# Kernel tuning notes

Hardware: AMD Instinct MI355X
Metric: run time of the kernel (lower is better)

## Reference

```python
import jax, jax.numpy as jnp
import numpy as np
import math

H = 12
DH = 64
MAX_POS = 1024

def setup_inputs() -> dict:
    key = jax.random.key(0)
    ks = jax.random.split(key, 8)
    B, L, D = 2, 1024, 768
    s = 0.02
    return {
        "hidden_states": jax.random.normal(ks[0], (B, L, D), jnp.float32),
        "attention_mask": jnp.zeros((B, 1, 1, L), jnp.float32),
        "struct_matrix": jax.random.uniform(ks[1], (5, B, 1, L, L), jnp.float32),
        "Wq": jax.random.normal(ks[2], (D, D), jnp.float32) * s,
        "bq": jnp.zeros((D,), jnp.float32),
        "Wk": jax.random.normal(ks[3], (D, D), jnp.float32) * s,
        "bk": jnp.zeros((D,), jnp.float32),
        "Wv": jax.random.normal(ks[4], (D, D), jnp.float32) * s,
        "bv": jnp.zeros((D,), jnp.float32),
        "dist_emb": jax.random.normal(ks[5], (2 * MAX_POS - 1, DH), jnp.float32) * s,
        "ssan_w": jax.random.normal(ks[6], (5, H, DH, DH), jnp.float32) * s,
        "abs_bias": jnp.zeros((5, H), jnp.float32),
    }

def reference(hidden_states, attention_mask, struct_matrix, Wq, bq, Wk, bk, Wv, bv, dist_emb, ssan_w, abs_bias):
    B, L, D = hidden_states.shape

    def heads(x):  # [B,L,D] -> [B,H,L,dh]
        return x.reshape(B, L, H, DH).transpose(0, 2, 1, 3)

    q = heads(hidden_states @ Wq + bq)
    k = heads(hidden_states @ Wk + bk)
    v = heads(hidden_states @ Wv + bv)

    scores = jnp.einsum('bhqd,bhkd->bhqk', q, k)

    # relative_key_query positional scores
    pos_ids = jnp.arange(L)
    distance = pos_ids[:, None] - pos_ids[None, :]          # [L,L]
    pos = dist_emb[distance + MAX_POS - 1]                  # [L,L,dh]
    scores = scores + jnp.einsum('bhld,lrd->bhlr', q, pos)
    scores = scores + jnp.einsum('bhrd,lrd->bhlr', k, pos)

    scores = scores / math.sqrt(DH)
    scores = scores + attention_mask

    # 5 SSAN bilinear bias terms, masked by structural matrices
    for i in range(5):
        bias = jnp.einsum('bhqd,hde,bhke->bhqk', q, ssan_w[i], k)
        scores = scores + (bias + abs_bias[i][None, :, None, None]) * struct_matrix[i]

    probs = jax.nn.softmax(scores, axis=-1)
    ctx = jnp.einsum('bhqk,bhkd->bqhd', probs, v).reshape(B, L, D)
    return ctx
```

## Files before the change

kernel.cpp:

```cpp
#include <hip/hip_runtime.h>
#include <math.h>

#define NB 2
#define NL 1024
#define ND 768
#define NH 12
#define DH 64

typedef _Float16 f16;
typedef _Float16 f16x2 __attribute__((ext_vector_type(2)));
typedef _Float16 f16x4 __attribute__((ext_vector_type(4)));
typedef _Float16 f16x8 __attribute__((ext_vector_type(8)));
typedef float f32x4 __attribute__((ext_vector_type(4)));

#define MFMA16(a, b, c) __builtin_amdgcn_mfma_f32_16x16x32_f16((a), (b), (c), 0, 0, 0)

__device__ __forceinline__ void soft_barrier() {
    asm volatile("s_waitcnt lgkmcnt(0)\n\ts_barrier" ::: "memory");
}

__global__ __launch_bounds__(256) void prep_kernel(
    const float* __restrict__ hs,
    const float* __restrict__ Wq, const float* __restrict__ Wk,
    const float* __restrict__ Wv, const float* __restrict__ sw,
    const float* __restrict__ de,
    f16* __restrict__ hsf, f16* __restrict__ wt, f16* __restrict__ swt,
    f16* __restrict__ de16)
{
    __shared__ float sT[64 * 66];
    const int t = threadIdx.x;
    const int tile = blockIdx.x;

    if (tile < 768) {
        const int base = tile * 2048 + t * 8;
        float4 a = *(const float4*)&hs[base];
        float4 b = *(const float4*)&hs[base + 4];
        f16x8 hv;
        hv[0] = (f16)a.x; hv[1] = (f16)a.y; hv[2] = (f16)a.z; hv[3] = (f16)a.w;
        hv[4] = (f16)b.x; hv[5] = (f16)b.y; hv[6] = (f16)b.z; hv[7] = (f16)b.w;
        *(f16x8*)&hsf[base] = hv;
        return;
    }
    if (tile >= 1260) {
        const int base = (tile - 1260) * 2048 + t * 8;
        if (base < 2047 * 64) {
            float4 a = *(const float4*)&de[base];
            float4 b = *(const float4*)&de[base + 4];
            f16x8 hv;
            hv[0] = (f16)a.x; hv[1] = (f16)a.y; hv[2] = (f16)a.z; hv[3] = (f16)a.w;
            hv[4] = (f16)b.x; hv[5] = (f16)b.y; hv[6] = (f16)b.z; hv[7] = (f16)b.w;
            *(f16x8*)&de16[base] = hv;
        }
        return;
    }

    const float* S; f16* D; int sRS, dRS;
    const int ti = tile - 768;
    if (ti < 432) {
        const int mat = ti / 144, r2 = ti % 144, ht = r2 / 12, kt = r2 % 12;
        const float* W = (mat == 0) ? Wq : (mat == 1) ? Wk : Wv;
        S = W + (size_t)(kt * 64) * ND + ht * 64;
        D = wt + (size_t)((mat * NH + ht) * 64) * ND + kt * 64;
        sRS = ND; dRS = ND;
    } else {
        const int i = ti - 432;
        S = sw + (size_t)i * 4096;
        D = swt + (size_t)i * 4096;
        sRS = 64; dRS = 64;
    }

    {
        const int kk = t >> 2, nb = (t & 3) * 16;
        float v[16];
        #pragma unroll
        for (int j = 0; j < 4; ++j)
            *(float4*)&v[4 * j] = *(const float4*)&S[(size_t)kk * sRS + nb + 4 * j];
        #pragma unroll
        for (int jj = 0; jj < 16; ++jj)
            sT[(nb + jj) * 66 + kk] = v[jj];
    }
    soft_barrier();
    {
        const int n = t >> 2, kb = (t & 3) * 16;
        f16 tmp[16];
        #pragma unroll
        for (int j = 0; j < 8; ++j) {
            float2 x = *(float2*)&sT[n * 66 + kb + 2 * j];
            tmp[2 * j]     = (f16)x.x;
            tmp[2 * j + 1] = (f16)x.y;
        }
        *(f16x8*)&D[(size_t)n * dRS + kb]     = *(f16x8*)&tmp[0];
        *(f16x8*)&D[(size_t)n * dRS + kb + 8] = *(f16x8*)&tmp[8];
    }
}

__global__ __launch_bounds__(256, 4) void qkv_kernel(
    const f16* __restrict__ hsf, const f16* __restrict__ wt,
    const float* __restrict__ bq, const float* __restrict__ bk,
    const float* __restrict__ bv,
    f16* __restrict__ qf, f16* __restrict__ kf, f16* __restrict__ vt)
{
    __shared__ f16 sA[64 * 72], sB[64 * 72];
    __shared__ float sT[64 * 66];

    const int m0  = blockIdx.x * 64;
    const int y   = blockIdx.y;
    const int mat = y / NH, h = y % NH;
    const int t = threadIdx.x, lane = t & 63, w = t >> 6;
    const int quad = lane >> 4, l15 = lane & 15;
    const int wm = w >> 1, wn = w & 1;

    const float* bias = (mat == 0) ? bq : (mat == 1) ? bk : bv;

    f32x4 acc[2][2];
    #pragma unroll
    for (int r = 0; r < 2; ++r)
        #pragma unroll
        for (int c = 0; c < 2; ++c) acc[r][c] = (f32x4){0.f, 0.f, 0.f, 0.f};

    const int srow = t >> 2, scol = (t & 3) * 16;
    const f16* Ag = hsf + (size_t)(m0 + srow) * ND + scol;
    const f16* Bg = wt + ((size_t)y * 64 + srow) * ND + scol;

    for (int k0 = 0; k0 < ND; k0 += 64) {
        soft_barrier();
        *(f16x8*)&sA[srow * 72 + scol]     = *(const f16x8*)&Ag[k0];
        *(f16x8*)&sA[srow * 72 + scol + 8] = *(const f16x8*)&Ag[k0 + 8];
        *(f16x8*)&sB[srow * 72 + scol]     = *(const f16x8*)&Bg[k0];
        *(f16x8*)&sB[srow * 72 + scol + 8] = *(const f16x8*)&Bg[k0 + 8];
        soft_barrier();
        #pragma unroll
        for (int kk = 0; kk < 64; kk += 32) {
            const int ko = kk + quad * 8;
            f16x8 a0 = *(f16x8*)&sA[(32 * wm + l15) * 72 + ko];
            f16x8 a1 = *(f16x8*)&sA[(32 * wm + 16 + l15) * 72 + ko];
            f16x8 b0 = *(f16x8*)&sB[(32 * wn + l15) * 72 + ko];
            f16x8 b1 = *(f16x8*)&sB[(32 * wn + 16 + l15) * 72 + ko];
            acc[0][0] = MFMA16(a0, b0, acc[0][0]);
            acc[0][1] = MFMA16(a0, b1, acc[0][1]);
            acc[1][0] = MFMA16(a1, b0, acc[1][0]);
            acc[1][1] = MFMA16(a1, b1, acc[1][1]);
        }
    }
    soft_barrier();

    const int bb = m0 >> 10;
    const int lbase = m0 & 1023;
    const int bh = bb * NH + h;

    if (mat < 2) {
        #pragma unroll
        for (int r = 0; r < 2; ++r)
            #pragma unroll
            for (int c = 0; c < 2; ++c) {
                const int col = 32 * wn + 16 * c + l15;
                const float bz = bias[h * 64 + col];
                #pragma unroll
                for (int rr = 0; rr < 4; ++rr)
                    sT[(32 * wm + 16 * r + 4 * quad + rr) * 66 + col] = acc[r][c][rr] + bz;
            }
        soft_barrier();
        const int orow = t >> 2, ocb = (t & 3) * 16;
        f16 tmp[16];
        #pragma unroll
        for (int j = 0; j < 8; ++j) {
            float2 x = *(float2*)&sT[orow * 66 + ocb + 2 * j];
            tmp[2 * j] = (f16)x.x; tmp[2 * j + 1] = (f16)x.y;
        }
        f16* dst = ((mat == 0) ? qf : kf) + ((size_t)bh * NL + lbase + orow) * DH + ocb;
        *(f16x8*)dst       = *(f16x8*)&tmp[0];
        *(f16x8*)(dst + 8) = *(f16x8*)&tmp[8];
    } else {
        #pragma unroll
        for (int r = 0; r < 2; ++r)
            #pragma unroll
            for (int c = 0; c < 2; ++c) {
                const int col = 32 * wn + 16 * c + l15;
                const float bz = bias[h * 64 + col];
                #pragma unroll
                for (int rr = 0; rr < 4; ++rr)
                    sT[col * 66 + 32 * wm + 16 * r + 4 * quad + rr] = acc[r][c][rr] + bz;
            }
        soft_barrier();
        const int d = t >> 2, lcb = (t & 3) * 16;
        f16 tmp[16];
        #pragma unroll
        for (int j = 0; j < 8; ++j) {
            float2 x = *(float2*)&sT[d * 66 + lcb + 2 * j];
            tmp[2 * j] = (f16)x.x; tmp[2 * j + 1] = (f16)x.y;
        }
        f16* dst = vt + ((size_t)bh * DH + d) * NL + lbase + lcb;
        *(f16x8*)dst       = *(f16x8*)&tmp[0];
        *(f16x8*)(dst + 8) = *(f16x8*)&tmp[8];
    }
}

__global__ __launch_bounds__(256, 2) void attn_kernel(
    const f16* __restrict__ qf, const f16* __restrict__ kf,
    const f16* __restrict__ vt, const f16* __restrict__ swt,
    const float* __restrict__ mask, const float* __restrict__ struct_m,
    const f16* __restrict__ de16, const float* __restrict__ abs_bias,
    float* __restrict__ out)
{
    __shared__ f16 sK[64 * 72];
    __shared__ f16 sVt[2][64 * 72];
    __shared__ f16 sE[96 * 72];
    __shared__ f16 sQEl[96 * 34];
    __shared__ f16 sKEl[96 * 34];
    __shared__ float sS[32 * 68];
    __shared__ f16 sP[32 * 72];
    __shared__ float sAlpha[32], sL[32];

    const int l0 = blockIdx.x * 32;
    const int bh = blockIdx.y;
    const int bb = bh / NH, h = bh % NH;
    const int t  = threadIdx.x;
    const int lane  = t & 63;
    const int w     = t >> 6;
    const int quad  = lane >> 4;
    const int l15   = lane & 15;
    const int msub  = w >> 1;
    const int npair = w & 1;

    f16x8 aQ[2], aW[5][2];
    {
        const size_t qrow = ((size_t)bh * NL + l0 + 16 * msub + l15) * DH;
        #pragma unroll
        for (int K = 0; K < 2; ++K)
            aQ[K] = *(const f16x8*)&qf[qrow + 32 * K + 8 * quad];
    }

    {
        #pragma unroll
        for (int b = 0; b < 2; ++b) {
            const int pb0  = (b == 0) ? 0 : 3;
            const int pcnt = (b == 0) ? 3 : 2;
            #pragma unroll
            for (int pi = 0; pi < 3; ++pi) {
                if (pi < pcnt) {
                    const int p = pb0 + pi;
                    const f16* Wp = swt + ((size_t)(p * NH + h)) * 64 * 64;
                    #pragma unroll
                    for (int ntl = 0; ntl < 2; ++ntl) {
                        const int nt = 2 * npair + ntl;
                        f32x4 c = (f32x4){0.f, 0.f, 0.f, 0.f};
                        #pragma unroll
                        for (int K = 0; K < 2; ++K) {
                            f16x8 bw = *(const f16x8*)&Wp[(size_t)(16 * nt + l15) * 64 + 32 * K + 8 * quad];
                            c = MFMA16(aQ[K], bw, c);
                        }
                        #pragma unroll
                        for (int r = 0; r < 4; ++r)
                            sE[(pi * 32 + 16 * msub + 4 * quad + r) * 72 + 16 * nt + l15] = (f16)c[r];
                    }
                }
            }
            soft_barrier();
            #pragma unroll
            for (int pi = 0; pi < 3; ++pi) {
                if (pi < pcnt) {
                    #pragma unroll
                    for (int K = 0; K < 2; ++K)
                        aW[pb0 + pi][K] =
                            *(const f16x8*)&sE[(pi * 32 + 16 * msub + l15) * 72 + 32 * K + 8 * quad];
                }
            }
            soft_barrier();
        }
    }

    float ab[5];
    #pragma unroll
    for (int p = 0; p < 5; ++p) ab[p] = abs_bias[p * NH + h];

    float pf_st[5][2][4], pf_mask[2];

    auto stage_kv = [&](int r0s, int buf) {
        const int row = t >> 3, col = (t & 7) * 8;
        const f16* ks = kf + ((size_t)bh * NL + r0s) * DH;
        *(f16x8*)&sK[row * 72 + col]        = *(const f16x8*)&ks[row * 64 + col];
        *(f16x8*)&sK[(row + 32) * 72 + col] = *(const f16x8*)&ks[(row + 32) * 64 + col];
        const f16* vs = vt + (size_t)bh * DH * NL + r0s;
        *(f16x8*)&sVt[buf][row * 72 + col] =
            *(const f16x8*)&vs[(size_t)row * NL + col];
        *(f16x8*)&sVt[buf][(row + 32) * 72 + col] =
            *(const f16x8*)&vs[(size_t)(row + 32) * NL + col];
    };
    auto stage_E = [&](int r0s) {
        const int ebase = l0 - r0s + 960;
        #pragma unroll
        for (int p2 = 0; p2 < 3; ++p2) {
            const int idx = t + 256 * p2;
            const int er = idx >> 3, col = (idx & 7) * 8;
            if (er < 95)
                *(f16x8*)&sE[er * 72 + col] =
                    *(const f16x8*)&de16[(size_t)(ebase + er) * DH + col];
        }
    };
    auto prefetch = [&](int r0s) {
        #pragma unroll
        for (int n = 0; n < 2; ++n) {
            const int j = 32 * npair + 16 * n + l15;
            pf_mask[n] = mask[bb * NL + r0s + j];
            #pragma unroll
            for (int r = 0; r < 4; ++r) {
                const int i = 16 * msub + 4 * quad + r;
                #pragma unroll
                for (int p = 0; p < 5; ++p)
                    pf_st[p][n][r] =
                        struct_m[((size_t)(p * NB + bb) * NL + l0 + i) * NL + r0s + j];
            }
        }
    };

    stage_kv(0, 0);
    stage_E(0);
    prefetch(0);

    const int sm_i = t >> 3;
    const int sm_jb = t & 7;
    float m_cur = -INFINITY, l_cur = 0.f;
    f32x4 O[2];
    O[0] = (f32x4){0.f, 0.f, 0.f, 0.f};
    O[1] = (f32x4){0.f, 0.f, 0.f, 0.f};

    for (int kt = 0; kt < 16; ++kt) {
        const int cur = kt & 1;
        soft_barrier();

        {
            const int krow = (16 * w + l15) * 72;
            f16x8 ak0 = *(f16x8*)&sK[krow + quad * 8];
            f16x8 ak1 = *(f16x8*)&sK[krow + 32 + quad * 8];
            #pragma unroll
            for (int c = 0; c < 3; ++c) {
                const int nt = 3 - w + c;
                const int erow = (16 * nt + l15) * 72;
                f16x8 e0 = *(f16x8*)&sE[erow + quad * 8];
                f16x8 e1 = *(f16x8*)&sE[erow + 32 + quad * 8];
                f32x4 ck = (f32x4){0.f, 0.f, 0.f, 0.f};
                ck = MFMA16(ak0, e0, ck);
                ck = MFMA16(ak1, e1, ck);
                const int base = (16 * nt + l15) * 34 + 16 * w + 4 * quad;
                f16x2 lo = {(f16)ck[0], (f16)ck[1]};
                f16x2 hi = {(f16)ck[2], (f16)ck[3]};
                *(f16x2*)&sKEl[base]     = lo;
                *(f16x2*)&sKEl[base + 2] = hi;
            }
            const int qs = 3 * npair + msub;
            const int qc = 3 - npair;
            #pragma unroll
            for (int c = 0; c < 3; ++c) {
                if (c < qc) {
                    const int nt = qs + c;
                    const int erow = (16 * nt + l15) * 72;
                    f16x8 e0 = *(f16x8*)&sE[erow + quad * 8];
                    f16x8 e1 = *(f16x8*)&sE[erow + 32 + quad * 8];
                    f32x4 cq = (f32x4){0.f, 0.f, 0.f, 0.f};
                    cq = MFMA16(aQ[0], e0, cq);
                    cq = MFMA16(aQ[1], e1, cq);
                    const int base = (16 * nt + l15) * 34 + 16 * msub + 4 * quad;
                    f16x2 lo = {(f16)cq[0], (f16)cq[1]};
                    f16x2 hi = {(f16)cq[2], (f16)cq[3]};
                    *(f16x2*)&sQEl[base]     = lo;
                    *(f16x2*)&sQEl[base + 2] = hi;
                }
            }
        }
        soft_barrier();

        {
            f32x4 acc[2][6];
            #pragma unroll
            for (int n = 0; n < 2; ++n)
                #pragma unroll
                for (int p = 0; p < 6; ++p)
                    acc[n][p] = (f32x4){0.f, 0.f, 0.f, 0.f};

            #pragma unroll
            for (int K = 0; K < 2; ++K) {
                const int koff = K * 32 + quad * 8;
                f16x8 bk2[2];
                #pragma unroll
                for (int n = 0; n < 2; ++n)
                    bk2[n] = *(f16x8*)&sK[(32 * npair + 16 * n + l15) * 72 + koff];
                #pragma unroll
                for (int n = 0; n < 2; ++n)
                    acc[n][0] = MFMA16(aQ[K], bk2[n], acc[n][0]);
                #pragma unroll
                for (int p = 0; p < 5; ++p)
                    #pragma unroll
                    for (int n = 0; n < 2; ++n)
                        acc[n][1 + p] = MFMA16(aW[p][K], bk2[n], acc[n][1 + p]);
            }

            #pragma unroll
            for (int n = 0; n < 2; ++n) {
                const int j = 32 * npair + 16 * n + l15;
                #pragma unroll
                for (int r = 0; r < 4; ++r) {
                    const int i = 16 * msub + 4 * quad + r;
                    const int tp = i - j + 63;
                    float posv = (float)sQEl[tp * 34 + i] + (float)sKEl[tp * 34 + j];
                    float s = (acc[n][0][r] + posv) * 0.125f + pf_mask[n];
                    #pragma unroll
                    for (int p = 0; p < 5; ++p)
                        s += (acc[n][1 + p][r] + ab[p]) * pf_st[p][n][r];
                    sS[i * 68 + j] = s;
                }
            }
        }
        soft_barrier();

        {
            float sv[8];
            float smax = -INFINITY;
            #pragma unroll
            for (int k = 0; k < 8; ++k) {
                sv[k] = sS[sm_i * 68 + sm_jb + 8 * k];
                smax = fmaxf(smax, sv[k]);
            }
            #pragma unroll
            for (int off = 4; off > 0; off >>= 1)
                smax = fmaxf(smax, __shfl_xor(smax, off, 8));
            const float m_new = fmaxf(m_cur, smax);
            const float alpha = __expf(m_cur - m_new);
            float rsum = 0.f;
            #pragma unroll
            for (int k = 0; k < 8; ++k) {
                float p = __expf(sv[k] - m_new);
                sP[sm_i * 72 + sm_jb + 8 * k] = (f16)p;
                rsum += p;
            }
            #pragma unroll
            for (int off = 4; off > 0; off >>= 1)
                rsum += __shfl_xor(rsum, off, 8);
            l_cur = l_cur * alpha + rsum;
            m_cur = m_new;
            if (sm_jb == 0) { sAlpha[sm_i] = alpha; sL[sm_i] = l_cur; }
        }
        soft_barrier();

        {
            if (kt < 15) {
                stage_kv((kt + 1) * 64, cur ^ 1);
                stage_E((kt + 1) * 64);
                prefetch((kt + 1) * 64);
            }

            float a4[4];
            #pragma unroll
            for (int r = 0; r < 4; ++r) a4[r] = sAlpha[16 * msub + 4 * quad + r];
            #pragma unroll
            for (int n = 0; n < 2; ++n)
                #pragma unroll
                for (int r = 0; r < 4; ++r) O[n][r] *= a4[r];

            const int prow = (16 * msub + l15) * 72;
            #pragma unroll
            for (int K = 0; K < 2; ++K) {
                const int koff = K * 32 + quad * 8;
                f16x8 pfr = *(f16x8*)&sP[prow + koff];
                #pragma unroll
                for (int n = 0; n < 2; ++n) {
                    f16x8 vfr = *(f16x8*)&sVt[cur][(32 * npair + 16 * n + l15) * 72 + koff];
                    O[n] = MFMA16(pfr, vfr, O[n]);
                }
            }
        }
    }

    float linv[4];
    #pragma unroll
    for (int r = 0; r < 4; ++r) linv[r] = 1.0f / sL[16 * msub + 4 * quad + r];
    #pragma unroll
    for (int n = 0; n < 2; ++n) {
        const int dh = 32 * npair + 16 * n + l15;
        #pragma unroll
        for (int r = 0; r < 4; ++r) {
            const int i = 16 * msub + 4 * quad + r;
            out[((size_t)bb * NL + l0 + i) * ND + h * DH + dh] = O[n][r] * linv[r];
        }
    }
}

extern "C" void kernel_launch(void* const* d_in, const int* in_sizes, int n_in,
                              void* d_out, int out_size, void* d_ws, size_t ws_size,
                              hipStream_t stream) {
    const float* hs   = (const float*)d_in[0];
    const float* mask = (const float*)d_in[1];
    const float* stm  = (const float*)d_in[2];
    const float* Wq   = (const float*)d_in[3];
    const float* bq   = (const float*)d_in[4];
    const float* Wk   = (const float*)d_in[5];
    const float* bk   = (const float*)d_in[6];
    const float* Wv   = (const float*)d_in[7];
    const float* bv   = (const float*)d_in[8];
    const float* de   = (const float*)d_in[9];
    const float* sw   = (const float*)d_in[10];
    const float* abb  = (const float*)d_in[11];
    float* outp = (float*)d_out;

    const size_t NQKV = (size_t)NB * NH * NL * DH;
    char* ws = (char*)d_ws;
    f16* qf   = (f16*)ws;                 ws += NQKV * 2;
    f16* kf   = (f16*)ws;                 ws += NQKV * 2;
    f16* vtb  = (f16*)ws;                 ws += NQKV * 2;
    f16* hsf  = (f16*)ws;                 ws += NQKV * 2;
    f16* wt   = (f16*)ws;                 ws += (size_t)2304 * 768 * 2;
    f16* swt  = (f16*)ws;                 ws += (size_t)245760 * 2;
    f16* de16 = (f16*)ws;

    prep_kernel<<<1324, 256, 0, stream>>>(hs, Wq, Wk, Wv, sw, de,
                                          hsf, wt, swt, de16);
    qkv_kernel<<<dim3(32, 36), 256, 0, stream>>>(hsf, wt, bq, bk, bv, qf, kf, vtb);
    attn_kernel<<<dim3(32, 24), 256, 0, stream>>>(qf, kf, vtb, swt,
                                                  mask, stm, de16, abb, outp);
}
```

Baseline: 230.9 us.

## Fuse hidden-state fp16 cast into QKV GEMM and register-stage attention K/V/E loads

Removes the separate fp32-to-fp16 conversion of hidden_states from the prep kernel. The QKV GEMM now reads fp32 directly and converts while filling shared memory, which drops one global round trip and shrinks the prep grid. The attention kernel splits K/V/E staging into a global load into registers issued before the score computation and a later shared-memory write after softmax. This hides global latency behind compute and removes one barrier per iteration. In exchange the QKV kernel re-reads fp32 A tiles 36 times, which doubles A-side traffic, and the held registers may lower occupancy.

```diff
diff --git a/kernel.cpp b/kernel.cpp
--- a/kernel.cpp
+++ b/kernel.cpp
@@ -20,29 +20,17 @@
 }
 
 __global__ __launch_bounds__(256) void prep_kernel(
-    const float* __restrict__ hs,
     const float* __restrict__ Wq, const float* __restrict__ Wk,
     const float* __restrict__ Wv, const float* __restrict__ sw,
     const float* __restrict__ de,
-    f16* __restrict__ hsf, f16* __restrict__ wt, f16* __restrict__ swt,
-    f16* __restrict__ de16)
+    f16* __restrict__ wt, f16* __restrict__ swt, f16* __restrict__ de16)
 {
     __shared__ float sT[64 * 66];
     const int t = threadIdx.x;
     const int tile = blockIdx.x;
 
-    if (tile < 768) {
-        const int base = tile * 2048 + t * 8;
-        float4 a = *(const float4*)&hs[base];
-        float4 b = *(const float4*)&hs[base + 4];
-        f16x8 hv;
-        hv[0] = (f16)a.x; hv[1] = (f16)a.y; hv[2] = (f16)a.z; hv[3] = (f16)a.w;
-        hv[4] = (f16)b.x; hv[5] = (f16)b.y; hv[6] = (f16)b.z; hv[7] = (f16)b.w;
-        *(f16x8*)&hsf[base] = hv;
-        return;
-    }
-    if (tile >= 1260) {
-        const int base = (tile - 1260) * 2048 + t * 8;
+    if (tile >= 492) {
+        const int base = (tile - 492) * 2048 + t * 8;
         if (base < 2047 * 64) {
             float4 a = *(const float4*)&de[base];
             float4 b = *(const float4*)&de[base + 4];
@@ -55,15 +43,14 @@
     }
 
     const float* S; f16* D; int sRS, dRS;
-    const int ti = tile - 768;
-    if (ti < 432) {
-        const int mat = ti / 144, r2 = ti % 144, ht = r2 / 12, kt = r2 % 12;
+    if (tile < 432) {
+        const int mat = tile / 144, r2 = tile % 144, ht = r2 / 12, kt = r2 % 12;
         const float* W = (mat == 0) ? Wq : (mat == 1) ? Wk : Wv;
         S = W + (size_t)(kt * 64) * ND + ht * 64;
         D = wt + (size_t)((mat * NH + ht) * 64) * ND + kt * 64;
         sRS = ND; dRS = ND;
     } else {
-        const int i = ti - 432;
+        const int i = tile - 432;
         S = sw + (size_t)i * 4096;
         D = swt + (size_t)i * 4096;
         sRS = 64; dRS = 64;
@@ -95,7 +82,7 @@
 }
 
 __global__ __launch_bounds__(256, 4) void qkv_kernel(
-    const f16* __restrict__ hsf, const f16* __restrict__ wt,
+    const float* __restrict__ hs, const f16* __restrict__ wt,
     const float* __restrict__ bq, const float* __restrict__ bk,
     const float* __restrict__ bv,
     f16* __restrict__ qf, f16* __restrict__ kf, f16* __restrict__ vt)
@@ -119,13 +106,24 @@
         for (int c = 0; c < 2; ++c) acc[r][c] = (f32x4){0.f, 0.f, 0.f, 0.f};
 
     const int srow = t >> 2, scol = (t & 3) * 16;
-    const f16* Ag = hsf + (size_t)(m0 + srow) * ND + scol;
+    const float* Ag = hs + (size_t)(m0 + srow) * ND + scol;
     const f16* Bg = wt + ((size_t)y * 64 + srow) * ND + scol;
 
     for (int k0 = 0; k0 < ND; k0 += 64) {
         soft_barrier();
-        *(f16x8*)&sA[srow * 72 + scol]     = *(const f16x8*)&Ag[k0];
-        *(f16x8*)&sA[srow * 72 + scol + 8] = *(const f16x8*)&Ag[k0 + 8];
+        {
+            float4 a0 = *(const float4*)&Ag[k0];
+            float4 a1 = *(const float4*)&Ag[k0 + 4];
+            float4 a2 = *(const float4*)&Ag[k0 + 8];
+            float4 a3 = *(const float4*)&Ag[k0 + 12];
+            f16x8 ha, hb;
+            ha[0] = (f16)a0.x; ha[1] = (f16)a0.y; ha[2] = (f16)a0.z; ha[3] = (f16)a0.w;
+            ha[4] = (f16)a1.x; ha[5] = (f16)a1.y; ha[6] = (f16)a1.z; ha[7] = (f16)a1.w;
+            hb[0] = (f16)a2.x; hb[1] = (f16)a2.y; hb[2] = (f16)a2.z; hb[3] = (f16)a2.w;
+            hb[4] = (f16)a3.x; hb[5] = (f16)a3.y; hb[6] = (f16)a3.z; hb[7] = (f16)a3.w;
+            *(f16x8*)&sA[srow * 72 + scol]     = ha;
+            *(f16x8*)&sA[srow * 72 + scol + 8] = hb;
+        }
         *(f16x8*)&sB[srow * 72 + scol]     = *(const f16x8*)&Bg[k0];
         *(f16x8*)&sB[srow * 72 + scol + 8] = *(const f16x8*)&Bg[k0 + 8];
         soft_barrier();
@@ -274,27 +272,41 @@
     for (int p = 0; p < 5; ++p) ab[p] = abs_bias[p * NH + h];
 
     float pf_st[5][2][4], pf_mask[2];
-
-    auto stage_kv = [&](int r0s, int buf) {
+    f16x8 kreg[2], vreg[2], ereg[3];
+
+    auto issue_kv = [&](int r0s) {
         const int row = t >> 3, col = (t & 7) * 8;
         const f16* ks = kf + ((size_t)bh * NL + r0s) * DH;
-        *(f16x8*)&sK[row * 72 + col]        = *(const f16x8*)&ks[row * 64 + col];
-        *(f16x8*)&sK[(row + 32) * 72 + col] = *(const f16x8*)&ks[(row + 32) * 64 + col];
+        kreg[0] = *(const f16x8*)&ks[row * 64 + col];
+        kreg[1] = *(const f16x8*)&ks[(row + 32) * 64 + col];
         const f16* vs = vt + (size_t)bh * DH * NL + r0s;
-        *(f16x8*)&sVt[buf][row * 72 + col] =
-            *(const f16x8*)&vs[(size_t)row * NL + col];
-        *(f16x8*)&sVt[buf][(row + 32) * 72 + col] =
-            *(const f16x8*)&vs[(size_t)(row + 32) * NL + col];
+        vreg[0] = *(const f16x8*)&vs[(size_t)row * NL + col];
+        vreg[1] = *(const f16x8*)&vs[(size_t)(row + 32) * NL + col];
     };
-    auto stage_E = [&](int r0s) {
+    auto write_kv = [&](int buf) {
+        const int row = t >> 3, col = (t & 7) * 8;
+        *(f16x8*)&sK[row * 72 + col]             = kreg[0];
+        *(f16x8*)&sK[(row + 32) * 72 + col]      = kreg[1];
+        *(f16x8*)&sVt[buf][row * 72 + col]       = vreg[0];
+        *(f16x8*)&sVt[buf][(row + 32) * 72 + col] = vreg[1];
+    };
+    auto issue_E = [&](int r0s) {
         const int ebase = l0 - r0s + 960;
         #pragma unroll
         for (int p2 = 0; p2 < 3; ++p2) {
             const int idx = t + 256 * p2;
-            const int er = idx >> 3, col = (idx & 7) * 8;
+            const int er = idx >> 3, colE = (idx & 7) * 8;
             if (er < 95)
-                *(f16x8*)&sE[er * 72 + col] =
-                    *(const f16x8*)&de16[(size_t)(ebase + er) * DH + col];
+                ereg[p2] = *(const f16x8*)&de16[(size_t)(ebase + er) * DH + colE];
+        }
+    };
+    auto write_E = [&]() {
+        #pragma unroll
+        for (int p2 = 0; p2 < 3; ++p2) {
+            const int idx = t + 256 * p2;
+            const int er = idx >> 3, colE = (idx & 7) * 8;
+            if (er < 95)
+                *(f16x8*)&sE[er * 72 + colE] = ereg[p2];
         }
     };
     auto prefetch = [&](int r0s) {
@@ -313,8 +325,10 @@
         }
     };
 
-    stage_kv(0, 0);
-    stage_E(0);
+    issue_kv(0);
+    issue_E(0);
+    write_kv(0);
+    write_E();
     prefetch(0);
 
     const int sm_i = t >> 3;
@@ -324,9 +338,10 @@
     O[0] = (f32x4){0.f, 0.f, 0.f, 0.f};
     O[1] = (f32x4){0.f, 0.f, 0.f, 0.f};
 
+    soft_barrier();
+
     for (int kt = 0; kt < 16; ++kt) {
         const int cur = kt & 1;
-        soft_barrier();
 
         {
             const int krow = (16 * w + l15) * 72;
@@ -370,6 +385,11 @@
         soft_barrier();
 
         {
+            if (kt < 15) {
+                issue_kv((kt + 1) * 64);
+                issue_E((kt + 1) * 64);
+            }
+
             f32x4 acc[2][6];
             #pragma unroll
             for (int n = 0; n < 2; ++n)
@@ -438,16 +458,16 @@
             l_cur = l_cur * alpha + rsum;
             m_cur = m_new;
             if (sm_jb == 0) { sAlpha[sm_i] = alpha; sL[sm_i] = l_cur; }
+
+            if (kt < 15) {
+                write_kv(cur ^ 1);
+                write_E();
+                prefetch((kt + 1) * 64);
+            }
         }
         soft_barrier();
 
         {
-            if (kt < 15) {
-                stage_kv((kt + 1) * 64, cur ^ 1);
-                stage_E((kt + 1) * 64);
-                prefetch((kt + 1) * 64);
-            }
-
             float a4[4];
             #pragma unroll
             for (int r = 0; r < 4; ++r) a4[r] = sAlpha[16 * msub + 4 * quad + r];
@@ -506,14 +526,12 @@
     f16* qf   = (f16*)ws;                 ws += NQKV * 2;
     f16* kf   = (f16*)ws;                 ws += NQKV * 2;
     f16* vtb  = (f16*)ws;                 ws += NQKV * 2;
-    f16* hsf  = (f16*)ws;                 ws += NQKV * 2;
     f16* wt   = (f16*)ws;                 ws += (size_t)2304 * 768 * 2;
     f16* swt  = (f16*)ws;                 ws += (size_t)245760 * 2;
     f16* de16 = (f16*)ws;
 
-    prep_kernel<<<1324, 256, 0, stream>>>(hs, Wq, Wk, Wv, sw, de,
-                                          hsf, wt, swt, de16);
-    qkv_kernel<<<dim3(32, 36), 256, 0, stream>>>(hsf, wt, bq, bk, bv, qf, kf, vtb);
+    prep_kernel<<<556, 256, 0, stream>>>(Wq, Wk, Wv, sw, de, wt, swt, de16);
+    qkv_kernel<<<dim3(32, 36), 256, 0, stream>>>(hs, wt, bq, bk, bv, qf, kf, vtb);
     attn_kernel<<<dim3(32, 24), 256, 0, stream>>>(qf, kf, vtb, swt,
                                                   mask, stm, de16, abb, outp);
 }
```

Measured after the change: 220.0 us. -4.7%, faster.
